# Kernel optimization log

Measured on AMD Instinct MI355X. Metric: run time of the kernel, lower is better.

Reference implementation:

```python
import jax, jax.numpy as jnp
import numpy as np

N = 100000      # nodes
E = 1600000     # edges
F_IN = 128
HID = 64
N_CLS = 40


def setup_inputs() -> dict:
    key = jax.random.key(0)
    ks = jax.random.split(key, 8)
    x = jax.random.normal(ks[0], (N, F_IN), dtype=jnp.float32)
    edge_index = jax.random.randint(ks[1], (2, E), 0, N, dtype=jnp.int64)
    # SAGEConv params: lin_l (applied to mean-aggregated neighbors, with bias),
    # lin_r (applied to root/self features, no bias). Glorot-ish init scaling.
    W1_l = jax.random.normal(ks[2], (F_IN, HID), dtype=jnp.float32) / np.sqrt(F_IN)
    b1 = jnp.zeros((HID,), dtype=jnp.float32)
    W1_r = jax.random.normal(ks[3], (F_IN, HID), dtype=jnp.float32) / np.sqrt(F_IN)
    W2_l = jax.random.normal(ks[4], (HID, N_CLS), dtype=jnp.float32) / np.sqrt(HID)
    b2 = jnp.zeros((N_CLS,), dtype=jnp.float32)
    W2_r = jax.random.normal(ks[5], (HID, N_CLS), dtype=jnp.float32) / np.sqrt(HID)
    return {"x": x, "edge_index": edge_index,
            "W1_l": W1_l, "b1": b1, "W1_r": W1_r,
            "W2_l": W2_l, "b2": b2, "W2_r": W2_r}


def _sage_conv(x, src, dst, W_l, b_l, W_r):
    # mean aggregation of neighbor features: messages flow src -> dst
    msgs = x[src]                                              # [E, d]
    summed = jax.ops.segment_sum(msgs, dst, num_segments=N)    # [N, d]
    cnt = jax.ops.segment_sum(jnp.ones((src.shape[0],), x.dtype), dst,
                              num_segments=N)                  # [N]
    agg = summed / jnp.maximum(cnt, 1.0)[:, None]
    return agg @ W_l + b_l + x @ W_r


def reference(x, edge_index, W1_l, b1, W1_r, W2_l, b2, W2_r):
    src, dst = edge_index[0], edge_index[1]
    h = jax.nn.relu(_sage_conv(x, src, dst, W1_l, b1, W1_r))
    # dropout: identity in eval mode
    logits = _sage_conv(h, src, dst, W2_l, b2, W2_r)
    return jax.nn.log_softmax(logits, axis=1)
```

## Files before the change

### kernel.cpp

```cpp
#include <hip/hip_runtime.h>
#include <math.h>

#define N_NODES 100000
#define F_IN    128
#define HID     64
#define N_CLS   40
#define MT      (N_NODES / 16)

#define BSHIFT  9
#define BSZ     512
#define NB      ((N_NODES + BSZ - 1) / BSZ)
#define EPB     4096

typedef __attribute__((ext_vector_type(8))) short bf8_t;
typedef __attribute__((ext_vector_type(4))) float f4_t;
typedef __attribute__((ext_vector_type(2))) float f2v_t;

typedef unsigned short ushort_t;
typedef unsigned int uint_t;
typedef unsigned char uchar_t;

__device__ __forceinline__ ushort_t f2b(float f) {
    union { float f; uint_t u; } c; c.f = f;
    uint_t u = c.u + 0x7FFFu + ((c.u >> 16) & 1u);
    return (ushort_t)(u >> 16);
}
__device__ __forceinline__ float b2f(ushort_t h) {
    union { uint_t u; float f; } c; c.u = ((uint_t)h) << 16;
    return c.f;
}

#if defined(__has_builtin)
#if __has_builtin(__builtin_amdgcn_cvt_pk_f32_fp8) && __has_builtin(__builtin_amdgcn_cvt_pk_fp8_f32)
#define HAVE_FP8_HW 1
#endif
#endif

__device__ __forceinline__ uchar_t fp8_enc(float v) {
#ifdef HAVE_FP8_HW
    return (uchar_t)(__builtin_amdgcn_cvt_pk_fp8_f32(v, v, 0, false) & 0xff);
#else
    union { float f; uint_t u; } c; c.f = v;
    uint_t s = c.u >> 31;
    float av = fabsf(v);
    if (av > 448.f) av = 448.f;
    int e;
    float m = frexpf(av, &e);
    int ee = e + 6;
    uchar_t r;
    if (av == 0.f) r = 0;
    else if (ee <= 0) {
        int q = (int)(av * 512.f + 0.5f);
        if (q > 7) q = 7;
        r = (uchar_t)q;
    } else {
        int q = (int)(m * 16.f + 0.5f);
        if (q == 16) { q = 8; ee += 1; }
        if (ee > 15) { ee = 15; q = 15; }
        r = (uchar_t)((ee << 3) | (q & 7));
    }
    return r | (uchar_t)(s << 7);
#endif
}

__device__ __forceinline__ f2v_t fp8x2_dec_lo(uint_t w) {
#ifdef HAVE_FP8_HW
    return __builtin_amdgcn_cvt_pk_f32_fp8(w, false);
#else
    f2v_t r;
    for (int k = 0; k < 2; ++k) {
        uchar_t b = (w >> (8 * k)) & 0xff;
        uint_t s = (b >> 7) & 1, e = (b >> 3) & 15, m = b & 7;
        float f;
        if (e) { union { uint_t u; float ff; } c;
                 c.u = (s << 31) | ((e + 120) << 23) | (m << 20); f = c.ff; }
        else   { f = (float)m * 0.001953125f; if (s) f = -f; }
        r[k] = f;
    }
    return r;
#endif
}
__device__ __forceinline__ f2v_t fp8x2_dec_hi(uint_t w) {
#ifdef HAVE_FP8_HW
    return __builtin_amdgcn_cvt_pk_f32_fp8(w, true);
#else
    return fp8x2_dec_lo(w >> 16);
#endif
}

__global__ void block_hist_kernel(const int* __restrict__ ei, int E,
                                  int* __restrict__ blockHist) {
    __shared__ int cnt[NB];
    int t = threadIdx.x, blk = blockIdx.x;
    for (int i = t; i < NB; i += 256) cnt[i] = 0;
    __syncthreads();
    int e0 = blk * EPB;
#pragma unroll
    for (int i = 0; i < EPB / 256; ++i) {
        int e = e0 + i * 256 + t;
        if (e < E) atomicAdd(&cnt[ei[E + e] >> BSHIFT], 1);
    }
    __syncthreads();
    for (int i = t; i < NB; i += 256) blockHist[blk * NB + i] = cnt[i];
}

__global__ void col_scan_kernel(const int* __restrict__ blockHist, int nblk,
                                int* __restrict__ blockBase,
                                int* __restrict__ btot) {
    __shared__ int ss[256];
    __shared__ int carry;
    int bin = blockIdx.x, t = threadIdx.x;
    if (t == 0) carry = 0;
    __syncthreads();
    for (int c0 = 0; c0 < nblk; c0 += 256) {
        int b = c0 + t;
        int v = (b < nblk) ? blockHist[b * NB + bin] : 0;
        ss[t] = v;
        __syncthreads();
        for (int off = 1; off < 256; off <<= 1) {
            int u = (t >= off) ? ss[t - off] : 0;
            __syncthreads();
            ss[t] += u;
            __syncthreads();
        }
        if (b < nblk) blockBase[b * NB + bin] = carry + ss[t] - v;
        __syncthreads();
        if (t == 255) carry += ss[255];
        __syncthreads();
    }
    if (t == 0) btot[bin] = carry;
}

__global__ void scatter_pairs_kernel(const int* __restrict__ ei, int E,
                                     const int* __restrict__ blockBase,
                                     const int* __restrict__ btot,
                                     uint_t* __restrict__ pairs) {
    __shared__ int cur[NB];
    __shared__ int base[NB];
    __shared__ int ss[256];
    int t = threadIdx.x, blk = blockIdx.x;
    int v = (t < NB) ? btot[t] : 0;
    ss[t] = v;
    __syncthreads();
    for (int off = 1; off < 256; off <<= 1) {
        int u = (t >= off) ? ss[t - off] : 0;
        __syncthreads();
        ss[t] += u;
        __syncthreads();
    }
    if (t < NB) {
        cur[t] = 0;
        base[t] = (ss[t] - v) + blockBase[blk * NB + t];
    }
    __syncthreads();
    int e0 = blk * EPB;
#pragma unroll
    for (int i = 0; i < EPB / 256; ++i) {
        int e = e0 + i * 256 + t;
        if (e < E) {
            int src = ei[e];
            int dst = ei[E + e];
            int bin = dst >> BSHIFT;
            int r = atomicAdd(&cur[bin], 1);
            pairs[base[bin] + r] = ((uint_t)src << BSHIFT) | (uint_t)(dst & (BSZ - 1));
        }
    }
}

__global__ void bucket_sort_kernel(const uint_t* __restrict__ pairs,
                                   const int* __restrict__ btot,
                                   int* __restrict__ rowptr,
                                   int* __restrict__ csr) {
    __shared__ int hist[BSZ];
    __shared__ int lofs[BSZ];
    int bin = blockIdx.x, t = threadIdx.x;
    int pv = (t < NB) ? btot[t] : 0;
    lofs[t] = pv;
    __syncthreads();
    for (int off = 1; off < BSZ; off <<= 1) {
        int u = (t >= off) ? lofs[t - off] : 0;
        __syncthreads();
        lofs[t] += u;
        __syncthreads();
    }
    int base = (bin > 0) ? lofs[bin - 1] : 0;
    int cnt = btot[bin];
    __syncthreads();
    hist[t] = 0;
    __syncthreads();
    for (int i = t; i < cnt; i += BSZ)
        atomicAdd(&hist[pairs[base + i] & (BSZ - 1)], 1);
    __syncthreads();
    int v = hist[t];
    lofs[t] = v;
    __syncthreads();
    for (int off = 1; off < BSZ; off <<= 1) {
        int u = (t >= off) ? lofs[t - off] : 0;
        __syncthreads();
        lofs[t] += u;
        __syncthreads();
    }
    int excl = lofs[t] - v;
    int d_global = (bin << BSHIFT) + t;
    if (d_global < N_NODES) rowptr[d_global] = base + excl;
    if (bin == NB - 1 && t == 0) rowptr[N_NODES] = base + cnt;
    __syncthreads();
    lofs[t] = excl;
    hist[t] = 0;
    __syncthreads();
    for (int i = t; i < cnt; i += BSZ) {
        uint_t p = pairs[base + i];
        int lb = p & (BSZ - 1);
        int r = atomicAdd(&hist[lb], 1);
        csr[base + lofs[lb] + r] = (int)(p >> BSHIFT);
    }
}

__global__ void cvt_w_kernel(const float* __restrict__ W1l,
                             const float* __restrict__ W1r,
                             const float* __restrict__ W2l,
                             const float* __restrict__ W2r,
                             ushort_t* __restrict__ W1t,
                             ushort_t* __restrict__ W2t) {
    int t = blockIdx.x * blockDim.x + threadIdx.x;
    if (t < 128 * F_IN) {
        int n = t / F_IN, k = t - n * F_IN;
        float v = (n < HID) ? W1l[k * HID + n] : W1r[k * HID + (n - HID)];
        W1t[t] = f2b(v);
    } else if (t < 128 * F_IN + 80 * HID) {
        int u = t - 128 * F_IN;
        int n = u / HID, k = u - n * HID;
        float v = (n < N_CLS) ? W2l[k * N_CLS + n] : W2r[k * N_CLS + (n - N_CLS)];
        W2t[u] = f2b(v);
    }
}

__global__ void gemm1_mfma_kernel(const float* __restrict__ x,
                                  const ushort_t* __restrict__ W1t,
                                  uchar_t* __restrict__ y1f8,
                                  ushort_t* __restrict__ z1b) {
    __shared__ uchar_t sy[128][80];
    __shared__ ushort_t sz[128][72];
    int tid = threadIdx.x;
    int wave = tid >> 6, lane = tid & 63;
    int tile0 = blockIdx.x * 8 + wave * 2;
    int m0b = blockIdx.x * 128;
    int r = lane & 15, q = lane >> 4;
    bool v0 = (tile0 < MT), v1 = (tile0 + 1 < MT);

    bf8_t a0[4], a1[4];
#pragma unroll
    for (int kt = 0; kt < 4; ++kt) { a0[kt] = (bf8_t)(short)0; a1[kt] = (bf8_t)(short)0; }
    if (v0) {
        const float* xr = x + (size_t)(tile0 * 16 + r) * F_IN + q * 8;
#pragma unroll
        for (int kt = 0; kt < 4; ++kt) {
            float4 u = *(const float4*)(xr + kt * 32);
            float4 v = *(const float4*)(xr + kt * 32 + 4);
            bf8_t tt;
            tt[0] = (short)f2b(u.x); tt[1] = (short)f2b(u.y);
            tt[2] = (short)f2b(u.z); tt[3] = (short)f2b(u.w);
            tt[4] = (short)f2b(v.x); tt[5] = (short)f2b(v.y);
            tt[6] = (short)f2b(v.z); tt[7] = (short)f2b(v.w);
            a0[kt] = tt;
        }
    }
    if (v1) {
        const float* xr = x + (size_t)((tile0 + 1) * 16 + r) * F_IN + q * 8;
#pragma unroll
        for (int kt = 0; kt < 4; ++kt) {
            float4 u = *(const float4*)(xr + kt * 32);
            float4 v = *(const float4*)(xr + kt * 32 + 4);
            bf8_t tt;
            tt[0] = (short)f2b(u.x); tt[1] = (short)f2b(u.y);
            tt[2] = (short)f2b(u.z); tt[3] = (short)f2b(u.w);
            tt[4] = (short)f2b(v.x); tt[5] = (short)f2b(v.y);
            tt[6] = (short)f2b(v.z); tt[7] = (short)f2b(v.w);
            a1[kt] = tt;
        }
    }
    int lr0 = wave * 32 + q * 4;
#pragma unroll
    for (int tn = 0; tn < 8; ++tn) {
        const ushort_t* wr = W1t + (size_t)(tn * 16 + r) * F_IN + q * 8;
        bf8_t b[4];
#pragma unroll
        for (int kt = 0; kt < 4; ++kt)
            b[kt] = *(const bf8_t*)(wr + kt * 32);
        f4_t acc0 = {0.f, 0.f, 0.f, 0.f};
        f4_t acc1 = {0.f, 0.f, 0.f, 0.f};
#pragma unroll
        for (int kt = 0; kt < 4; ++kt) {
            acc0 = __builtin_amdgcn_mfma_f32_16x16x32_bf16(a0[kt], b[kt], acc0, 0, 0, 0);
            acc1 = __builtin_amdgcn_mfma_f32_16x16x32_bf16(a1[kt], b[kt], acc1, 0, 0, 0);
        }
        int col = tn * 16 + r;
        if (col < 64) {
            if (v0) {
#pragma unroll
                for (int rr = 0; rr < 4; ++rr) sy[lr0 + rr][col] = fp8_enc(acc0[rr]);
            }
            if (v1) {
#pragma unroll
                for (int rr = 0; rr < 4; ++rr) sy[lr0 + 16 + rr][col] = fp8_enc(acc1[rr]);
            }
        } else {
            if (v0) {
#pragma unroll
                for (int rr = 0; rr < 4; ++rr) sz[lr0 + rr][col - 64] = f2b(acc0[rr]);
            }
            if (v1) {
#pragma unroll
                for (int rr = 0; rr < 4; ++rr) sz[lr0 + 16 + rr][col - 64] = f2b(acc1[rr]);
            }
        }
    }
    __syncthreads();
    int vrows = N_NODES - m0b; if (vrows > 128) vrows = 128;
    for (int idx = tid; idx < vrows * 4; idx += 256) {
        int row = idx >> 2, c = (idx & 3) << 4;
        *(uint4*)(y1f8 + (size_t)(m0b + row) * 64 + c) = *(const uint4*)&sy[row][c];
    }
    for (int idx = tid; idx < vrows * 8; idx += 256) {
        int row = idx >> 3, c = (idx & 7) << 3;
        *(uint4*)(z1b + (size_t)(m0b + row) * HID + c) = *(const uint4*)&sz[row][c];
    }
}

__device__ __forceinline__ void acc16(float* acc, uint4 v) {
    f2v_t p;
    p = fp8x2_dec_lo(v.x); acc[0]  += p[0]; acc[1]  += p[1];
    p = fp8x2_dec_hi(v.x); acc[2]  += p[0]; acc[3]  += p[1];
    p = fp8x2_dec_lo(v.y); acc[4]  += p[0]; acc[5]  += p[1];
    p = fp8x2_dec_hi(v.y); acc[6]  += p[0]; acc[7]  += p[1];
    p = fp8x2_dec_lo(v.z); acc[8]  += p[0]; acc[9]  += p[1];
    p = fp8x2_dec_hi(v.z); acc[10] += p[0]; acc[11] += p[1];
    p = fp8x2_dec_lo(v.w); acc[12] += p[0]; acc[13] += p[1];
    p = fp8x2_dec_hi(v.w); acc[14] += p[0]; acc[15] += p[1];
}

__global__ void agg1_kernel(const int* __restrict__ rowptr,
                            const int* __restrict__ csr,
                            const uchar_t* __restrict__ y1f8,
                            const ushort_t* __restrict__ z1b,
                            const float* __restrict__ b1,
                            ushort_t* __restrict__ hb,
                            uchar_t* __restrict__ hf8) {
    int gid = blockIdx.x * blockDim.x + threadIdx.x;
    int wave = gid >> 6, lane = gid & 63;
    int g = lane >> 2, l = lane & 3;
    int n = wave * 16 + g;
    if (n >= N_NODES) return;
    int beg = rowptr[n], end = rowptr[n + 1];
    float acc[16];
#pragma unroll
    for (int j = 0; j < 16; ++j) acc[j] = 0.f;
    const uchar_t* yb = y1f8 + l * 16;
    int i = beg;
    for (; i + 3 < end; i += 4) {
        int s0 = csr[i], s1 = csr[i + 1], s2 = csr[i + 2], s3 = csr[i + 3];
        uint4 w0 = *(const uint4*)(yb + (size_t)s0 * 64);
        uint4 w1 = *(const uint4*)(yb + (size_t)s1 * 64);
        uint4 w2 = *(const uint4*)(yb + (size_t)s2 * 64);
        uint4 w3 = *(const uint4*)(yb + (size_t)s3 * 64);
        acc16(acc, w0); acc16(acc, w1); acc16(acc, w2); acc16(acc, w3);
    }
    for (; i < end; ++i) {
        uint4 w = *(const uint4*)(yb + (size_t)csr[i] * 64);
        acc16(acc, w);
    }
    float inv = 1.0f / fmaxf((float)(end - beg), 1.0f);
    int c = l * 16;
    ushort_t zz[16];
    *(uint4*)&zz[0] = *(const uint4*)(z1b + (size_t)n * HID + c);
    *(uint4*)&zz[8] = *(const uint4*)(z1b + (size_t)n * HID + c + 8);
    float bv[16];
    *(float4*)&bv[0]  = *(const float4*)(b1 + c);
    *(float4*)&bv[4]  = *(const float4*)(b1 + c + 4);
    *(float4*)&bv[8]  = *(const float4*)(b1 + c + 8);
    *(float4*)&bv[12] = *(const float4*)(b1 + c + 12);
    ushort_t o[16];
    uchar_t of[16];
#pragma unroll
    for (int j = 0; j < 16; ++j) {
        float r = fmaxf(fmaf(acc[j], inv, bv[j] + b2f(zz[j])), 0.f);
        o[j] = f2b(r);
        of[j] = fp8_enc(r);
    }
    *(uint4*)(hb + (size_t)n * HID + c)     = *(const uint4*)&o[0];
    *(uint4*)(hb + (size_t)n * HID + c + 8) = *(const uint4*)&o[8];
    *(uint4*)(hf8 + (size_t)n * 64 + c)     = *(const uint4*)&of[0];
}

__global__ void layer2_fused_kernel(const int* __restrict__ rowptr,
                                    const int* __restrict__ csr,
                                    const uchar_t* __restrict__ hf8,
                                    const ushort_t* __restrict__ hb,
                                    const ushort_t* __restrict__ W2t,
                                    const float* __restrict__ b2,
                                    float* __restrict__ out) {
    __shared__ ushort_t sA[64][72];
    __shared__ float sO[64][44];
    int tid = threadIdx.x;
    int wave = tid >> 6, lane = tid & 63;
    int m0b = blockIdx.x * 64;
    int tileN = m0b + wave * 16;
    bool valid = (tileN < N_NODES);

    if (valid) {
        int g = lane >> 2, l = lane & 3;
        int n = tileN + g;
        int beg = rowptr[n], end = rowptr[n + 1];
        float acc[16];
#pragma unroll
        for (int j = 0; j < 16; ++j) acc[j] = 0.f;
        const uchar_t* yb = hf8 + l * 16;
        int i = beg;
        for (; i + 3 < end; i += 4) {
            int s0 = csr[i], s1 = csr[i + 1], s2 = csr[i + 2], s3 = csr[i + 3];
            uint4 w0 = *(const uint4*)(yb + (size_t)s0 * 64);
            uint4 w1 = *(const uint4*)(yb + (size_t)s1 * 64);
            uint4 w2 = *(const uint4*)(yb + (size_t)s2 * 64);
            uint4 w3 = *(const uint4*)(yb + (size_t)s3 * 64);
            acc16(acc, w0); acc16(acc, w1); acc16(acc, w2); acc16(acc, w3);
        }
        for (; i < end; ++i) {
            uint4 w = *(const uint4*)(yb + (size_t)csr[i] * 64);
            acc16(acc, w);
        }
        float inv = 1.0f / fmaxf((float)(end - beg), 1.0f);
        ushort_t o[16];
#pragma unroll
        for (int j = 0; j < 16; ++j)
            o[j] = f2b(acc[j] * inv);
        int lrow = wave * 16 + g;
        *(uint4*)&sA[lrow][l * 16]     = *(const uint4*)&o[0];
        *(uint4*)&sA[lrow][l * 16 + 8] = *(const uint4*)&o[8];
    }
    __syncthreads();
    if (valid) {
        int r = lane & 15, q = lane >> 4;
        const ushort_t* ar = &sA[wave * 16 + r][q * 8];
        const ushort_t* hr = hb + (size_t)(tileN + r) * HID + q * 8;
        bf8_t a0[2], a1[2];
#pragma unroll
        for (int kt = 0; kt < 2; ++kt) {
            a0[kt] = *(const bf8_t*)(ar + kt * 32);
            a1[kt] = *(const bf8_t*)(hr + kt * 32);
        }
        float v[3][4];
#pragma unroll
        for (int tn = 0; tn < 3; ++tn) {
            int col = tn * 16 + r;
            int cl = (col < N_CLS) ? col : 0;
            const ushort_t* wl  = W2t + (size_t)cl * HID + q * 8;
            const ushort_t* wr2 = W2t + (size_t)(N_CLS + cl) * HID + q * 8;
            f4_t acc4 = {0.f, 0.f, 0.f, 0.f};
#pragma unroll
            for (int kt = 0; kt < 2; ++kt) {
                bf8_t bl = *(const bf8_t*)(wl + kt * 32);
                acc4 = __builtin_amdgcn_mfma_f32_16x16x32_bf16(a0[kt], bl, acc4, 0, 0, 0);
            }
#pragma unroll
            for (int kt = 0; kt < 2; ++kt) {
                bf8_t br = *(const bf8_t*)(wr2 + kt * 32);
                acc4 = __builtin_amdgcn_mfma_f32_16x16x32_bf16(a1[kt], br, acc4, 0, 0, 0);
            }
            float bias = (col < N_CLS) ? b2[cl] : 0.f;
#pragma unroll
            for (int rr = 0; rr < 4; ++rr)
                v[tn][rr] = (col < N_CLS) ? (acc4[rr] + bias) : -INFINITY;
        }
        int lrow = wave * 16 + q * 4;
#pragma unroll
        for (int rr = 0; rr < 4; ++rr) {
            float m = fmaxf(fmaxf(v[0][rr], v[1][rr]), v[2][rr]);
#pragma unroll
            for (int off = 1; off < 16; off <<= 1)
                m = fmaxf(m, __shfl_xor(m, off, 64));
            float s = 0.f;
#pragma unroll
            for (int tn = 0; tn < 3; ++tn)
                if (v[tn][rr] > -INFINITY) s += expf(v[tn][rr] - m);
#pragma unroll
            for (int off = 1; off < 16; off <<= 1)
                s += __shfl_xor(s, off, 64);
            float ls = m + logf(s);
#pragma unroll
            for (int tn = 0; tn < 3; ++tn) {
                int col = tn * 16 + r;
                if (col < N_CLS)
                    sO[lrow + rr][col] = v[tn][rr] - ls;
            }
        }
    }
    __syncthreads();
    int vrows = N_NODES - m0b; if (vrows > 64) vrows = 64;
    for (int idx = tid; idx < vrows * 10; idx += 256) {
        int row = idx / 10, c = (idx - row * 10) * 4;
        *(float4*)(out + (size_t)(m0b + row) * N_CLS + c) = *(const float4*)&sO[row][c];
    }
}

extern "C" void kernel_launch(void* const* d_in, const int* in_sizes, int n_in,
                              void* d_out, int out_size, void* d_ws, size_t ws_size,
                              hipStream_t stream) {
    const float* x   = (const float*)d_in[0];
    const int*   ei  = (const int*)d_in[1];
    const float* W1l = (const float*)d_in[2];
    const float* b1  = (const float*)d_in[3];
    const float* W1r = (const float*)d_in[4];
    const float* W2l = (const float*)d_in[5];
    const float* b2  = (const float*)d_in[6];
    const float* W2r = (const float*)d_in[7];
    float* out = (float*)d_out;
    const int E = in_sizes[1] / 2;
    const int nblk = (E + EPB - 1) / EPB;

    char* p = (char*)d_ws;
    auto take = [&](size_t bytes) {
        char* q = p;
        p += (bytes + 15) & ~(size_t)15;
        return (void*)q;
    };
    int* rowptr     = (int*)take(sizeof(int) * (N_NODES + 4));
    int* blockHist  = (int*)take(sizeof(int) * (size_t)nblk * NB);
    int* blockBase  = (int*)take(sizeof(int) * (size_t)nblk * NB);
    int* btot       = (int*)take(sizeof(int) * NB);
    uint_t* pairs   = (uint_t*)take(sizeof(uint_t) * (size_t)E);
    int* csr        = (int*)take(sizeof(int) * (size_t)E);
    ushort_t* W1t   = (ushort_t*)take(sizeof(ushort_t) * 128 * F_IN);
    ushort_t* W2t   = (ushort_t*)take(sizeof(ushort_t) * 80 * HID);
    uchar_t* y1f8   = (uchar_t*)take(sizeof(uchar_t) * (size_t)N_NODES * 64);
    ushort_t* z1b   = (ushort_t*)take(sizeof(ushort_t) * (size_t)N_NODES * HID);
    ushort_t* hb    = (ushort_t*)take(sizeof(ushort_t) * (size_t)N_NODES * HID);
    uchar_t* hf8    = (uchar_t*)take(sizeof(uchar_t) * (size_t)N_NODES * 64);

    const int B = 256;

    block_hist_kernel<<<nblk, 256, 0, stream>>>(ei, E, blockHist);
    col_scan_kernel<<<NB, 256, 0, stream>>>(blockHist, nblk, blockBase, btot);
    scatter_pairs_kernel<<<nblk, 256, 0, stream>>>(ei, E, blockBase, btot, pairs);
    bucket_sort_kernel<<<NB, BSZ, 0, stream>>>(pairs, btot, rowptr, csr);

    cvt_w_kernel<<<(128 * F_IN + 80 * HID + B - 1) / B, B, 0, stream>>>(
        W1l, W1r, W2l, W2r, W1t, W2t);

    int gemm1_blocks = (MT + 7) / 8;
    int l2_blocks = (N_NODES + 63) / 64;
    int t_agg = (N_NODES / 16) * 64;

    gemm1_mfma_kernel<<<gemm1_blocks, B, 0, stream>>>(x, W1t, y1f8, z1b);
    agg1_kernel<<<(t_agg + B - 1) / B, B, 0, stream>>>(rowptr, csr, y1f8, z1b, b1, hb, hf8);
    layer2_fused_kernel<<<l2_blocks, B, 0, stream>>>(rowptr, csr, hf8, hb, W2t, b2, out);
}
```

Baseline: 227.7 us.

## Co-launch independent kernels and degree-sort nodes within buckets for agg1

Merges the histogram kernel with the weight conversion, and the column scan with the first GEMM, into combined grids dispatched by blockIdx. This cuts launch count and lets independent work overlap. The bucket sort also builds a per-bucket permutation ordering nodes by clamped in-degree, and agg1 processes nodes in that order so lanes in a wave have similar loop trip counts. The cost is an extra perm array read and gather indirection, plus larger shared memory for the scan blocks in the merged kernel.

```diff
diff --git a/kernel.cpp b/kernel.cpp
--- a/kernel.cpp
+++ b/kernel.cpp
@@ -88,47 +88,163 @@
 #endif
 }
 
-__global__ void block_hist_kernel(const int* __restrict__ ei, int E,
-                                  int* __restrict__ blockHist) {
+__global__ void hist_cvt_kernel(const int* __restrict__ ei, int E, int nblk,
+                                int* __restrict__ blockHist,
+                                const float* __restrict__ W1l,
+                                const float* __restrict__ W1r,
+                                const float* __restrict__ W2l,
+                                const float* __restrict__ W2r,
+                                ushort_t* __restrict__ W1t,
+                                ushort_t* __restrict__ W2t) {
     __shared__ int cnt[NB];
-    int t = threadIdx.x, blk = blockIdx.x;
-    for (int i = t; i < NB; i += 256) cnt[i] = 0;
-    __syncthreads();
-    int e0 = blk * EPB;
-#pragma unroll
-    for (int i = 0; i < EPB / 256; ++i) {
-        int e = e0 + i * 256 + t;
-        if (e < E) atomicAdd(&cnt[ei[E + e] >> BSHIFT], 1);
-    }
-    __syncthreads();
-    for (int i = t; i < NB; i += 256) blockHist[blk * NB + i] = cnt[i];
-}
-
-__global__ void col_scan_kernel(const int* __restrict__ blockHist, int nblk,
-                                int* __restrict__ blockBase,
-                                int* __restrict__ btot) {
+    int t = threadIdx.x;
+    if ((int)blockIdx.x < nblk) {
+        int blk = blockIdx.x;
+        for (int i = t; i < NB; i += 256) cnt[i] = 0;
+        __syncthreads();
+        int e0 = blk * EPB;
+#pragma unroll
+        for (int i = 0; i < EPB / 256; ++i) {
+            int e = e0 + i * 256 + t;
+            if (e < E) atomicAdd(&cnt[ei[E + e] >> BSHIFT], 1);
+        }
+        __syncthreads();
+        for (int i = t; i < NB; i += 256) blockHist[blk * NB + i] = cnt[i];
+    } else {
+        int u = (blockIdx.x - nblk) * 256 + t;
+        if (u < 128 * F_IN) {
+            int n = u / F_IN, k = u - n * F_IN;
+            float v = (n < HID) ? W1l[k * HID + n] : W1r[k * HID + (n - HID)];
+            W1t[u] = f2b(v);
+        } else if (u < 128 * F_IN + 80 * HID) {
+            int w = u - 128 * F_IN;
+            int n = w / HID, k = w - n * HID;
+            float v = (n < N_CLS) ? W2l[k * N_CLS + n] : W2r[k * N_CLS + (n - N_CLS)];
+            W2t[w] = f2b(v);
+        }
+    }
+}
+
+__global__ void scan_gemm1_kernel(const int* __restrict__ blockHist, int nblk,
+                                  int* __restrict__ blockBase,
+                                  int* __restrict__ btot,
+                                  const float* __restrict__ x,
+                                  const ushort_t* __restrict__ W1t,
+                                  uchar_t* __restrict__ y1f8,
+                                  ushort_t* __restrict__ z1b) {
     __shared__ int ss[256];
     __shared__ int carry;
-    int bin = blockIdx.x, t = threadIdx.x;
-    if (t == 0) carry = 0;
-    __syncthreads();
-    for (int c0 = 0; c0 < nblk; c0 += 256) {
-        int b = c0 + t;
-        int v = (b < nblk) ? blockHist[b * NB + bin] : 0;
-        ss[t] = v;
-        __syncthreads();
-        for (int off = 1; off < 256; off <<= 1) {
-            int u = (t >= off) ? ss[t - off] : 0;
+    __shared__ uchar_t sy[128][80];
+    __shared__ ushort_t sz[128][72];
+    int t = threadIdx.x;
+    if (blockIdx.x < NB) {
+        int bin = blockIdx.x;
+        if (t == 0) carry = 0;
+        __syncthreads();
+        for (int c0 = 0; c0 < nblk; c0 += 256) {
+            int b = c0 + t;
+            int v = (b < nblk) ? blockHist[b * NB + bin] : 0;
+            ss[t] = v;
             __syncthreads();
-            ss[t] += u;
+            for (int off = 1; off < 256; off <<= 1) {
+                int u = (t >= off) ? ss[t - off] : 0;
+                __syncthreads();
+                ss[t] += u;
+                __syncthreads();
+            }
+            if (b < nblk) blockBase[b * NB + bin] = carry + ss[t] - v;
             __syncthreads();
-        }
-        if (b < nblk) blockBase[b * NB + bin] = carry + ss[t] - v;
-        __syncthreads();
-        if (t == 255) carry += ss[255];
-        __syncthreads();
-    }
-    if (t == 0) btot[bin] = carry;
+            if (t == 255) carry += ss[255];
+            __syncthreads();
+        }
+        if (t == 0) btot[bin] = carry;
+        return;
+    }
+    int gblk = blockIdx.x - NB;
+    int tid = t;
+    int wave = tid >> 6, lane = tid & 63;
+    int tile0 = gblk * 8 + wave * 2;
+    int m0b = gblk * 128;
+    int r = lane & 15, q = lane >> 4;
+    bool v0 = (tile0 < MT), v1 = (tile0 + 1 < MT);
+
+    bf8_t a0[4], a1[4];
+#pragma unroll
+    for (int kt = 0; kt < 4; ++kt) { a0[kt] = (bf8_t)(short)0; a1[kt] = (bf8_t)(short)0; }
+    if (v0) {
+        const float* xr = x + (size_t)(tile0 * 16 + r) * F_IN + q * 8;
+#pragma unroll
+        for (int kt = 0; kt < 4; ++kt) {
+            float4 u = *(const float4*)(xr + kt * 32);
+            float4 v = *(const float4*)(xr + kt * 32 + 4);
+            bf8_t tt;
+            tt[0] = (short)f2b(u.x); tt[1] = (short)f2b(u.y);
+            tt[2] = (short)f2b(u.z); tt[3] = (short)f2b(u.w);
+            tt[4] = (short)f2b(v.x); tt[5] = (short)f2b(v.y);
+            tt[6] = (short)f2b(v.z); tt[7] = (short)f2b(v.w);
+            a0[kt] = tt;
+        }
+    }
+    if (v1) {
+        const float* xr = x + (size_t)((tile0 + 1) * 16 + r) * F_IN + q * 8;
+#pragma unroll
+        for (int kt = 0; kt < 4; ++kt) {
+            float4 u = *(const float4*)(xr + kt * 32);
+            float4 v = *(const float4*)(xr + kt * 32 + 4);
+            bf8_t tt;
+            tt[0] = (short)f2b(u.x); tt[1] = (short)f2b(u.y);
+            tt[2] = (short)f2b(u.z); tt[3] = (short)f2b(u.w);
+            tt[4] = (short)f2b(v.x); tt[5] = (short)f2b(v.y);
+            tt[6] = (short)f2b(v.z); tt[7] = (short)f2b(v.w);
+            a1[kt] = tt;
+        }
+    }
+    int lr0 = wave * 32 + q * 4;
+#pragma unroll
+    for (int tn = 0; tn < 8; ++tn) {
+        const ushort_t* wr = W1t + (size_t)(tn * 16 + r) * F_IN + q * 8;
+        bf8_t b[4];
+#pragma unroll
+        for (int kt = 0; kt < 4; ++kt)
+            b[kt] = *(const bf8_t*)(wr + kt * 32);
+        f4_t acc0 = {0.f, 0.f, 0.f, 0.f};
+        f4_t acc1 = {0.f, 0.f, 0.f, 0.f};
+#pragma unroll
+        for (int kt = 0; kt < 4; ++kt) {
+            acc0 = __builtin_amdgcn_mfma_f32_16x16x32_bf16(a0[kt], b[kt], acc0, 0, 0, 0);
+            acc1 = __builtin_amdgcn_mfma_f32_16x16x32_bf16(a1[kt], b[kt], acc1, 0, 0, 0);
+        }
+        int col = tn * 16 + r;
+        if (col < 64) {
+            if (v0) {
+#pragma unroll
+                for (int rr = 0; rr < 4; ++rr) sy[lr0 + rr][col] = fp8_enc(acc0[rr]);
+            }
+            if (v1) {
+#pragma unroll
+                for (int rr = 0; rr < 4; ++rr) sy[lr0 + 16 + rr][col] = fp8_enc(acc1[rr]);
+            }
+        } else {
+            if (v0) {
+#pragma unroll
+                for (int rr = 0; rr < 4; ++rr) sz[lr0 + rr][col - 64] = f2b(acc0[rr]);
+            }
+            if (v1) {
+#pragma unroll
+                for (int rr = 0; rr < 4; ++rr) sz[lr0 + 16 + rr][col - 64] = f2b(acc1[rr]);
+            }
+        }
+    }
+    __syncthreads();
+    int vrows = N_NODES - m0b; if (vrows > 128) vrows = 128;
+    for (int idx = tid; idx < vrows * 4; idx += 256) {
+        int row = idx >> 2, c = (idx & 3) << 4;
+        *(uint4*)(y1f8 + (size_t)(m0b + row) * 64 + c) = *(const uint4*)&sy[row][c];
+    }
+    for (int idx = tid; idx < vrows * 8; idx += 256) {
+        int row = idx >> 3, c = (idx & 7) << 3;
+        *(uint4*)(z1b + (size_t)(m0b + row) * HID + c) = *(const uint4*)&sz[row][c];
+    }
 }
 
 __global__ void scatter_pairs_kernel(const int* __restrict__ ei, int E,
@@ -170,9 +286,12 @@
 __global__ void bucket_sort_kernel(const uint_t* __restrict__ pairs,
                                    const int* __restrict__ btot,
                                    int* __restrict__ rowptr,
-                                   int* __restrict__ csr) {
+                                   int* __restrict__ csr,
+                                   int* __restrict__ perm) {
     __shared__ int hist[BSZ];
     __shared__ int lofs[BSZ];
+    __shared__ int dh[64];
+    __shared__ int dbase_s[64];
     int bin = blockIdx.x, t = threadIdx.x;
     int pv = (t < NB) ? btot[t] : 0;
     lofs[t] = pv;
@@ -214,116 +333,21 @@
         int r = atomicAdd(&hist[lb], 1);
         csr[base + lofs[lb] + r] = (int)(p >> BSHIFT);
     }
-}
-
-__global__ void cvt_w_kernel(const float* __restrict__ W1l,
-                             const float* __restrict__ W1r,
-                             const float* __restrict__ W2l,
-                             const float* __restrict__ W2r,
-                             ushort_t* __restrict__ W1t,
-                             ushort_t* __restrict__ W2t) {
-    int t = blockIdx.x * blockDim.x + threadIdx.x;
-    if (t < 128 * F_IN) {
-        int n = t / F_IN, k = t - n * F_IN;
-        float v = (n < HID) ? W1l[k * HID + n] : W1r[k * HID + (n - HID)];
-        W1t[t] = f2b(v);
-    } else if (t < 128 * F_IN + 80 * HID) {
-        int u = t - 128 * F_IN;
-        int n = u / HID, k = u - n * HID;
-        float v = (n < N_CLS) ? W2l[k * N_CLS + n] : W2r[k * N_CLS + (n - N_CLS)];
-        W2t[u] = f2b(v);
-    }
-}
-
-__global__ void gemm1_mfma_kernel(const float* __restrict__ x,
-                                  const ushort_t* __restrict__ W1t,
-                                  uchar_t* __restrict__ y1f8,
-                                  ushort_t* __restrict__ z1b) {
-    __shared__ uchar_t sy[128][80];
-    __shared__ ushort_t sz[128][72];
-    int tid = threadIdx.x;
-    int wave = tid >> 6, lane = tid & 63;
-    int tile0 = blockIdx.x * 8 + wave * 2;
-    int m0b = blockIdx.x * 128;
-    int r = lane & 15, q = lane >> 4;
-    bool v0 = (tile0 < MT), v1 = (tile0 + 1 < MT);
-
-    bf8_t a0[4], a1[4];
-#pragma unroll
-    for (int kt = 0; kt < 4; ++kt) { a0[kt] = (bf8_t)(short)0; a1[kt] = (bf8_t)(short)0; }
-    if (v0) {
-        const float* xr = x + (size_t)(tile0 * 16 + r) * F_IN + q * 8;
-#pragma unroll
-        for (int kt = 0; kt < 4; ++kt) {
-            float4 u = *(const float4*)(xr + kt * 32);
-            float4 v = *(const float4*)(xr + kt * 32 + 4);
-            bf8_t tt;
-            tt[0] = (short)f2b(u.x); tt[1] = (short)f2b(u.y);
-            tt[2] = (short)f2b(u.z); tt[3] = (short)f2b(u.w);
-            tt[4] = (short)f2b(v.x); tt[5] = (short)f2b(v.y);
-            tt[6] = (short)f2b(v.z); tt[7] = (short)f2b(v.w);
-            a0[kt] = tt;
-        }
-    }
-    if (v1) {
-        const float* xr = x + (size_t)((tile0 + 1) * 16 + r) * F_IN + q * 8;
-#pragma unroll
-        for (int kt = 0; kt < 4; ++kt) {
-            float4 u = *(const float4*)(xr + kt * 32);
-            float4 v = *(const float4*)(xr + kt * 32 + 4);
-            bf8_t tt;
-            tt[0] = (short)f2b(u.x); tt[1] = (short)f2b(u.y);
-            tt[2] = (short)f2b(u.z); tt[3] = (short)f2b(u.w);
-            tt[4] = (short)f2b(v.x); tt[5] = (short)f2b(v.y);
-            tt[6] = (short)f2b(v.z); tt[7] = (short)f2b(v.w);
-            a1[kt] = tt;
-        }
-    }
-    int lr0 = wave * 32 + q * 4;
-#pragma unroll
-    for (int tn = 0; tn < 8; ++tn) {
-        const ushort_t* wr = W1t + (size_t)(tn * 16 + r) * F_IN + q * 8;
-        bf8_t b[4];
-#pragma unroll
-        for (int kt = 0; kt < 4; ++kt)
-            b[kt] = *(const bf8_t*)(wr + kt * 32);
-        f4_t acc0 = {0.f, 0.f, 0.f, 0.f};
-        f4_t acc1 = {0.f, 0.f, 0.f, 0.f};
-#pragma unroll
-        for (int kt = 0; kt < 4; ++kt) {
-            acc0 = __builtin_amdgcn_mfma_f32_16x16x32_bf16(a0[kt], b[kt], acc0, 0, 0, 0);
-            acc1 = __builtin_amdgcn_mfma_f32_16x16x32_bf16(a1[kt], b[kt], acc1, 0, 0, 0);
-        }
-        int col = tn * 16 + r;
-        if (col < 64) {
-            if (v0) {
-#pragma unroll
-                for (int rr = 0; rr < 4; ++rr) sy[lr0 + rr][col] = fp8_enc(acc0[rr]);
-            }
-            if (v1) {
-#pragma unroll
-                for (int rr = 0; rr < 4; ++rr) sy[lr0 + 16 + rr][col] = fp8_enc(acc1[rr]);
-            }
-        } else {
-            if (v0) {
-#pragma unroll
-                for (int rr = 0; rr < 4; ++rr) sz[lr0 + rr][col - 64] = f2b(acc0[rr]);
-            }
-            if (v1) {
-#pragma unroll
-                for (int rr = 0; rr < 4; ++rr) sz[lr0 + 16 + rr][col - 64] = f2b(acc1[rr]);
-            }
-        }
-    }
-    __syncthreads();
-    int vrows = N_NODES - m0b; if (vrows > 128) vrows = 128;
-    for (int idx = tid; idx < vrows * 4; idx += 256) {
-        int row = idx >> 2, c = (idx & 3) << 4;
-        *(uint4*)(y1f8 + (size_t)(m0b + row) * 64 + c) = *(const uint4*)&sy[row][c];
-    }
-    for (int idx = tid; idx < vrows * 8; idx += 256) {
-        int row = idx >> 3, c = (idx & 7) << 3;
-        *(uint4*)(z1b + (size_t)(m0b + row) * HID + c) = *(const uint4*)&sz[row][c];
+    int dcl = (v > 63) ? 63 : v;
+    if (t < 64) dh[t] = 0;
+    __syncthreads();
+    if (d_global < N_NODES) atomicAdd(&dh[dcl], 1);
+    __syncthreads();
+    if (t == 0) {
+        int s = 0;
+        for (int i = 0; i < 64; ++i) { dbase_s[i] = s; s += dh[i]; }
+    }
+    __syncthreads();
+    if (t < 64) dh[t] = 0;
+    __syncthreads();
+    if (d_global < N_NODES) {
+        int rk = atomicAdd(&dh[dcl], 1);
+        perm[(bin << BSHIFT) + dbase_s[dcl] + rk] = d_global;
     }
 }
 
@@ -341,6 +365,7 @@
 
 __global__ void agg1_kernel(const int* __restrict__ rowptr,
                             const int* __restrict__ csr,
+                            const int* __restrict__ perm,
                             const uchar_t* __restrict__ y1f8,
                             const ushort_t* __restrict__ z1b,
                             const float* __restrict__ b1,
@@ -349,8 +374,9 @@
     int gid = blockIdx.x * blockDim.x + threadIdx.x;
     int wave = gid >> 6, lane = gid & 63;
     int g = lane >> 2, l = lane & 3;
-    int n = wave * 16 + g;
-    if (n >= N_NODES) return;
+    int idx = wave * 16 + g;
+    if (idx >= N_NODES) return;
+    int n = perm[idx];
     int beg = rowptr[n], end = rowptr[n + 1];
     float acc[16];
 #pragma unroll
@@ -529,6 +555,7 @@
     int* btot       = (int*)take(sizeof(int) * NB);
     uint_t* pairs   = (uint_t*)take(sizeof(uint_t) * (size_t)E);
     int* csr        = (int*)take(sizeof(int) * (size_t)E);
+    int* perm       = (int*)take(sizeof(int) * N_NODES);
     ushort_t* W1t   = (ushort_t*)take(sizeof(ushort_t) * 128 * F_IN);
     ushort_t* W2t   = (ushort_t*)take(sizeof(ushort_t) * 80 * HID);
     uchar_t* y1f8   = (uchar_t*)take(sizeof(uchar_t) * (size_t)N_NODES * 64);
@@ -538,19 +565,17 @@
 
     const int B = 256;
 
-    block_hist_kernel<<<nblk, 256, 0, stream>>>(ei, E, blockHist);
-    col_scan_kernel<<<NB, 256, 0, stream>>>(blockHist, nblk, blockBase, btot);
-    scatter_pairs_kernel<<<nblk, 256, 0, stream>>>(ei, E, blockBase, btot, pairs);
-    bucket_sort_kernel<<<NB, BSZ, 0, stream>>>(pairs, btot, rowptr, csr);
-
-    cvt_w_kernel<<<(128 * F_IN + 80 * HID + B - 1) / B, B, 0, stream>>>(
-        W1l, W1r, W2l, W2r, W1t, W2t);
-
+    int cvt_blocks = (128 * F_IN + 80 * HID + B - 1) / B;
     int gemm1_blocks = (MT + 7) / 8;
     int l2_blocks = (N_NODES + 63) / 64;
     int t_agg = (N_NODES / 16) * 64;
 
-    gemm1_mfma_kernel<<<gemm1_blocks, B, 0, stream>>>(x, W1t, y1f8, z1b);
-    agg1_kernel<<<(t_agg + B - 1) / B, B, 0, stream>>>(rowptr, csr, y1f8, z1b, b1, hb, hf8);
+    hist_cvt_kernel<<<nblk + cvt_blocks, B, 0, stream>>>(
+        ei, E, nblk, blockHist, W1l, W1r, W2l, W2r, W1t, W2t);
+    scan_gemm1_kernel<<<NB + gemm1_blocks, B, 0, stream>>>(
+        blockHist, nblk, blockBase, btot, x, W1t, y1f8, z1b);
+    scatter_pairs_kernel<<<nblk, 256, 0, stream>>>(ei, E, blockBase, btot, pairs);
+    bucket_sort_kernel<<<NB, BSZ, 0, stream>>>(pairs, btot, rowptr, csr, perm);
+    agg1_kernel<<<(t_agg + B - 1) / B, B, 0, stream>>>(rowptr, csr, perm, y1f8, z1b, b1, hb, hf8);
     layer2_fused_kernel<<<l2_blocks, B, 0, stream>>>(rowptr, csr, hf8, hb, W2t, b2, out);
 }
```

Result: slower. 239.2 us (+5.0%).
